# Kernel optimization log

Measured on AMD Instinct MI355X. Metric: run time of the kernel, lower is better.

The kernel has to match this reference:

```python
import jax, jax.numpy as jnp
import numpy as np

DIM = 64
PATCH = 8
KH = KW = 7
K = KH * KW
PAD = 3


def conv2d(x, w, pad):
    return jax.lax.conv_general_dilated(
        x, w, window_strides=(1, 1), padding=[(pad, pad), (pad, pad)],
        dimension_numbers=('NCHW', 'OIHW', 'NCHW'))


def deform_conv2d(x, offset, mask, weight):
    # torchvision modulated deformable conv v2, stride=1, dilation=1, pad=PAD
    B, C, H, W = x.shape
    off = offset.reshape(B, K, 2, H, W)  # channel pairs are (dy, dx)
    ky, kx = jnp.meshgrid(jnp.arange(KH), jnp.arange(KW), indexing='ij')
    ky = ky.reshape(K).astype(x.dtype)
    kx = kx.reshape(K).astype(x.dtype)
    hh = jnp.arange(H, dtype=x.dtype)
    ww = jnp.arange(W, dtype=x.dtype)
    # sampling locations: p0 - pad + p_k + offset, shape [B,K,H,W]
    y = hh[None, None, :, None] - PAD + ky[None, :, None, None] + off[:, :, 0]
    xx = ww[None, None, None, :] - PAD + kx[None, :, None, None] + off[:, :, 1]

    y0 = jnp.floor(y)
    x0 = jnp.floor(xx)
    wy = y - y0
    wx = xx - x0

    img_flat = x.reshape(B, C, H * W)

    def gather(yi, xi):
        valid = (yi >= 0) & (yi < H) & (xi >= 0) & (xi < W)
        yc = jnp.clip(yi, 0, H - 1).astype(jnp.int32)
        xc = jnp.clip(xi, 0, W - 1).astype(jnp.int32)
        lin = (yc * W + xc).reshape(B, -1)  # [B, K*H*W]
        v = jax.vmap(lambda im, idx: im[:, idx])(img_flat, lin)  # [B,C,K*H*W]
        v = v.reshape(B, C, K, H, W)
        return v * valid[:, None].astype(x.dtype)

    val = ((1 - wy) * (1 - wx))[:, None] * gather(y0, x0) \
        + ((1 - wy) * wx)[:, None] * gather(y0, x0 + 1) \
        + (wy * (1 - wx))[:, None] * gather(y0 + 1, x0) \
        + (wy * wx)[:, None] * gather(y0 + 1, x0 + 1)
    val = val * mask[:, None]  # modulation, [B,C,K,H,W]
    wf = weight.reshape(weight.shape[0], weight.shape[1], K)
    return jnp.einsum('bckhw,ock->bohw', val, wf)


def setup_inputs() -> dict:
    key = jax.random.key(0)
    ks = jax.random.split(key, 12)
    B, C, H, W = 1, DIM, 192, 192
    s = 0.05
    return {
        'enc': jax.random.normal(ks[0], (B, C, H, W), jnp.float32),
        'dec': jax.random.normal(ks[1], (B, C, H, W), jnp.float32),
        'inverse_offset': jax.random.normal(ks[2], (B, 2 * K, H, W), jnp.float32),
        'inverse_weight': jax.random.uniform(ks[3], (B, K, H, W), jnp.float32),
        'w_proj_in': jax.random.normal(ks[4], (C, C, 1, 1), jnp.float32) * s,
        'fft_w': 1.0 + 0.1 * jax.random.normal(ks[5], (C, 1, 1, PATCH, PATCH // 2 + 1), jnp.float32),
        'w_proj_out': jax.random.normal(ks[6], (2 * C, 2 * C, 1, 1), jnp.float32) * s,
        'w_deform': jax.random.normal(ks[7], (C, C, KH, KW), jnp.float32) * s,
        'w_conv1': jax.random.normal(ks[8], (C, C, 1, 1), jnp.float32) * s,
        'w_conv2': jax.random.normal(ks[9], (C, C, 3, 3), jnp.float32) * s,
    }


def reference(enc, dec, inverse_offset, inverse_weight, w_proj_in, fft_w,
              w_proj_out, w_deform, w_conv1, w_conv2):
    B, C, h, w = enc.shape
    reverse = deform_conv2d(enc, inverse_offset, inverse_weight, w_deform)
    reverse = conv2d(reverse, w_conv1, 0)

    e = conv2d(enc, w_proj_in, 0)
    # check_image_size: pad H,W to multiples of PATCH (no-op for 192)
    ph = (-h) % PATCH
    pw = (-w) % PATCH
    e = jnp.pad(e, ((0, 0), (0, 0), (0, ph), (0, pw)))
    Hp, Wp = h + ph, w + pw
    # [B,C,h',w',p1,p2]
    xp = e.reshape(B, C, Hp // PATCH, PATCH, Wp // PATCH, PATCH).transpose(0, 1, 2, 4, 3, 5)
    xf = jnp.fft.rfft2(xp.astype(jnp.float32)) * fft_w  # fft_w [C,1,1,8,5] broadcasts
    xp = jnp.fft.irfft2(xf, s=(PATCH, PATCH))
    e = xp.transpose(0, 1, 2, 4, 3, 5).reshape(B, C, Hp, Wp)[:, :, :h, :w]

    e = e + reverse
    e = conv2d(e, w_conv2, 1)
    feat = jnp.concatenate([e, dec], axis=1)
    feat = conv2d(feat, w_proj_out, 0)
    x1, x2 = jnp.split(feat, 2, axis=1)  # SimpleGate
    return x1 * x2
```

## Files before the change

kernel.cpp:

```cpp
#include <hip/hip_runtime.h>
#include <math.h>

#define CH    64
#define WW    192
#define HH    192
#define HWSZ  (192*192)
#define KK    49
#define ROWP  68
#define SROW  72
#define C3ROW 72
#define OROW  136

typedef __attribute__((ext_vector_type(8))) short     s16x8;
typedef __attribute__((ext_vector_type(8))) _Float16  h16x8;
typedef __attribute__((ext_vector_type(2))) _Float16  h16x2;
typedef __attribute__((ext_vector_type(2))) __fp16    fp16x2;
typedef __attribute__((ext_vector_type(4))) float     f32x4;

__device__ __forceinline__ unsigned short f2h(float f) {
    union { _Float16 h; unsigned short s; } u; u.h = (_Float16)f;
    return u.s;
}

__device__ __forceinline__ unsigned pkh(float lo, float hi) {
    union { fp16x2 h; unsigned u; } v;
    v.h = __builtin_amdgcn_cvt_pkrtz(lo, hi);
    return v.u;
}

__device__ __forceinline__ h16x2 cvt2h(float a) {
    union { fp16x2 h; h16x2 o; } v;
    v.h = __builtin_amdgcn_cvt_pkrtz(a, a);
    return v.o;
}

__device__ __forceinline__ h16x2 as_h2(unsigned u) {
    union { unsigned u; h16x2 h; } v; v.u = u; return v.h;
}

__device__ __forceinline__ unsigned as_u(h16x2 h) {
    union { h16x2 h; unsigned u; } v; v.h = h; return v.u;
}

__device__ const float c_cos8[8] = {
    1.f, 0.70710678118654752f, 0.f, -0.70710678118654752f,
   -1.f, -0.70710678118654752f, 0.f, 0.70710678118654752f };

__global__ __launch_bounds__(256) void k_prep(
    const float* __restrict__ fw,
    const float* __restrict__ wd,
    const float* __restrict__ w2,
    const float* __restrict__ wc1,
    const float* __restrict__ wpo,
    const float* __restrict__ wpi,
    float* __restrict__ krT,
    short* __restrict__ wA,
    short* __restrict__ w2A,
    short* __restrict__ wpoA,
    short* __restrict__ wpiA)
{
    int tid = blockIdx.x * blockDim.x + threadIdx.x;
    int nt  = gridDim.x * blockDim.x;
    for (int t = tid; t < 64 * 64; t += nt) {
        int uv = t >> 6, c = t & 63;
        int u = uv >> 3, v = uv & 7;
        float acc = 0.f;
        for (int ky = 0; ky < 8; ky++)
            for (int kx = 0; kx < 8; kx++) {
                float wv = (kx <= 4) ? fw[c * 40 + ky * 5 + kx]
                                     : fw[c * 40 + ((8 - ky) & 7) * 5 + (8 - kx)];
                acc += wv * c_cos8[(ky * u + kx * v) & 7];
            }
        krT[uv * 64 + c] = acc * (1.f / 64.f);
    }
    for (int t = tid; t < 9 * 4096; t += nt) {
        int tap = t / 4096, rem = t & 4095;
        int o = rem >> 6, c = rem & 63;
        float v = w2[(o * 64 + c) * 9 + tap];
        int fi = tap * 8 + (o >> 4) * 2 + (c >> 5);
        int ln = ((c >> 3) & 3) * 16 + (o & 15);
        w2A[fi * 512 + ln * 8 + (c & 7)] = (short)f2h(v);
    }
    for (int t = tid; t < 128 * 128; t += nt) {
        int o = t >> 7, c = t & 127;
        int fi = (o >> 4) * 4 + (c >> 5);
        int ln = ((c >> 3) & 3) * 16 + (o & 15);
        wpoA[fi * 512 + ln * 8 + (c & 7)] = (short)f2h(wpo[t]);
    }
    for (int t = tid; t < 64 * 64; t += nt) {
        int o = t >> 6, c = t & 63;
        int fi = (o >> 4) * 2 + (c >> 5);
        int ln = ((c >> 3) & 3) * 16 + (o & 15);
        wpiA[fi * 512 + ln * 8 + (c & 7)] = (short)f2h(wpi[t]);
    }

    __shared__ float wdk [64 * ROWP];
    __shared__ float wc1s[64 * ROWP];
    int k = blockIdx.x;
    int t = threadIdx.x;
#pragma unroll
    for (int r = 0; r < 16; r++) {
        int idx = t + r * 256;
        int o = idx >> 6, c = idx & 63;
        wdk [o * ROWP + c] = wd[(o * 64 + c) * KK + k];
        wc1s[o * ROWP + c] = wc1[o * 64 + c];
    }
    __syncthreads();

    int ot = (t >> 4) * 4, cb = (t & 15) * 4;
    float a[4][4];
#pragma unroll
    for (int i = 0; i < 4; i++)
#pragma unroll
        for (int j = 0; j < 4; j++) a[i][j] = 0.f;
    for (int o = 0; o < 64; o++) {
        float wv_[4], sv_[4];
#pragma unroll
        for (int i = 0; i < 4; i++) wv_[i] = wc1s[(ot + i) * ROWP + o];
#pragma unroll
        for (int j = 0; j < 4; j++) sv_[j] = wdk[o * ROWP + cb + j];
#pragma unroll
        for (int i = 0; i < 4; i++)
#pragma unroll
            for (int j = 0; j < 4; j++) a[i][j] += wv_[i] * sv_[j];
    }
#pragma unroll
    for (int i = 0; i < 4; i++)
#pragma unroll
        for (int j = 0; j < 4; j++) {
            int o2 = ot + i, c = cb + j;
            int tt = o2 >> 4, m = o2 & 15;
            int kt = c >> 5, q = (c >> 3) & 3, jj = c & 7;
            int ln = q * 16 + m;
            wA[(k * 8 + tt * 2 + kt) * 512 + ln * 8 + jj] = (short)f2h(a[i][j]);
        }
}

__global__ __launch_bounds__(256) void k_trans(
    const float* __restrict__ enc, unsigned short* __restrict__ encH)
{
    __shared__ float s[64 * 65];
    int t = threadIdx.x;
    int base = blockIdx.x * 64;
#pragma unroll
    for (int r = 0; r < 16; r++) {
        int idx = t + r * 256;
        int p = idx & 63, c = idx >> 6;
        s[p * 65 + c] = enc[c * HWSZ + base + p];
    }
    __syncthreads();
#pragma unroll
    for (int r = 0; r < 8; r++) {
        int idx = t + r * 256;
        int pr = idx & 31, p = idx >> 5;
        ((unsigned*)encH)[(base + p) * 32 + pr] =
            pkh(s[p * 65 + 2 * pr], s[p * 65 + 2 * pr + 1]);
    }
}

#define REDW 20

__global__ __launch_bounds__(256) void k_deform(
    const unsigned short* __restrict__ encH, const float* __restrict__ off,
    const float* __restrict__ msk, const short* __restrict__ wA,
    float* __restrict__ rev)
{
    __shared__ __align__(16) short sm[4][16 * SROW];
    __shared__ __align__(16) float red[2 * 64 * REDW];

    int t = threadIdx.x;
    int lane = t & 63, w = t >> 6;
    int b = blockIdx.x;
    int xcd = b & 7, blk = b >> 3;
    int gy  = xcd * 24 + blk / 12;
    int gx0 = (blk % 12) * 16;

    int sp = lane >> 2, g = lane & 3;
    int sgx  = gx0 + sp;
    int gp_s = gy * WW + sgx;
    int n = lane & 15, q = lane >> 4;
    short* smw = &sm[w][0];

    f32x4 acc[4];
#pragma unroll
    for (int ot = 0; ot < 4; ot++) acc[ot] = (f32x4){0.f, 0.f, 0.f, 0.f};

    int kstart = (w == 0) ? 0 : 13 + (w - 1) * 12;
    int kend   = (w == 0) ? 13 : kstart + 12;

    float dy = off[(2 * kstart) * HWSZ + gp_s];
    float dx = off[(2 * kstart + 1) * HWSZ + gp_s];
    float mm = msk[kstart * HWSZ + gp_s];

#pragma unroll 1
    for (int k = kstart; k < kend; k++) {
        int ky = k / 7, kx = k % 7;
        float y = (float)(gy  - 3 + ky) + dy;
        float x = (float)(sgx - 3 + kx) + dx;
        float y0f = floorf(y), x0f = floorf(x);
        float wy = y - y0f, wx = x - x0f;
        int iy0 = (int)y0f, ix0 = (int)x0f;
        int iy1 = iy0 + 1, ix1 = ix0 + 1;
        bool vy0 = (iy0 >= 0) & (iy0 < HH);
        bool vy1 = (iy1 >= 0) & (iy1 < HH);
        bool vx0 = (ix0 >= 0) & (ix0 < WW);
        bool vx1 = (ix1 >= 0) & (ix1 < WW);
        int iy0c = min(max(iy0, 0), HH - 1), iy1c = min(max(iy1, 0), HH - 1);
        int ix0c = min(max(ix0, 0), WW - 1), ix1c = min(max(ix1, 0), WW - 1);
        float a00 = (vy0 & vx0) ? (1.f - wy) * (1.f - wx) * mm : 0.f;
        float a01 = (vy0 & vx1) ? (1.f - wy) * wx * mm : 0.f;
        float a10 = (vy1 & vx0) ? wy * (1.f - wx) * mm : 0.f;
        float a11 = (vy1 & vx1) ? wy * wx * mm : 0.f;

        const unsigned short* b00p = encH + (iy0c * WW + ix0c) * 64 + g * 8;
        const unsigned short* b01p = encH + (iy0c * WW + ix1c) * 64 + g * 8;
        const unsigned short* b10p = encH + (iy1c * WW + ix0c) * 64 + g * 8;
        const unsigned short* b11p = encH + (iy1c * WW + ix1c) * 64 + g * 8;
        uint4 u00[2], u01[2], u10[2], u11[2];
        u00[0] = *(const uint4*)b00p;  u00[1] = *(const uint4*)(b00p + 32);
        u01[0] = *(const uint4*)b01p;  u01[1] = *(const uint4*)(b01p + 32);
        u10[0] = *(const uint4*)b10p;  u10[1] = *(const uint4*)(b10p + 32);
        u11[0] = *(const uint4*)b11p;  u11[1] = *(const uint4*)(b11p + 32);

        float dyn = 0.f, dxn = 0.f, mmn = 0.f;
        if (k + 1 < kend) {
            dyn = off[(2 * k + 2) * HWSZ + gp_s];
            dxn = off[(2 * k + 3) * HWSZ + gp_s];
            mmn = msk[(k + 1) * HWSZ + gp_s];
        }

        h16x8 af[8];
#pragma unroll
        for (int f = 0; f < 8; f++)
            af[f] = *(const h16x8*)&wA[(k * 8 + f) * 512 + lane * 8];

        h16x2 w00 = cvt2h(a00);
        h16x2 w01 = cvt2h(a01);
        h16x2 w10 = cvt2h(a10);
        h16x2 w11 = cvt2h(a11);

        unsigned c00[8] = {u00[0].x, u00[0].y, u00[0].z, u00[0].w,
                           u00[1].x, u00[1].y, u00[1].z, u00[1].w};
        unsigned c01[8] = {u01[0].x, u01[0].y, u01[0].z, u01[0].w,
                           u01[1].x, u01[1].y, u01[1].z, u01[1].w};
        unsigned c10[8] = {u10[0].x, u10[0].y, u10[0].z, u10[0].w,
                           u10[1].x, u10[1].y, u10[1].z, u10[1].w};
        unsigned c11[8] = {u11[0].x, u11[0].y, u11[0].z, u11[0].w,
                           u11[1].x, u11[1].y, u11[1].z, u11[1].w};
        unsigned pk[8];
#pragma unroll
        for (int j = 0; j < 8; j++) {
            h16x2 r = as_h2(c00[j]) * w00;
            r = as_h2(c01[j]) * w01 + r;
            r = as_h2(c10[j]) * w10 + r;
            r = as_h2(c11[j]) * w11 + r;
            pk[j] = as_u(r);
        }
        *(uint4*)&smw[sp * SROW + g * 8]      = make_uint4(pk[0], pk[1], pk[2], pk[3]);
        *(uint4*)&smw[sp * SROW + 32 + g * 8] = make_uint4(pk[4], pk[5], pk[6], pk[7]);

        h16x8 b0 = *(const h16x8*)&smw[n * SROW +  0 + q * 8];
        h16x8 b1 = *(const h16x8*)&smw[n * SROW + 32 + q * 8];

#pragma unroll
        for (int ot = 0; ot < 4; ot++) {
            acc[ot] = __builtin_amdgcn_mfma_f32_16x16x32_f16(af[ot * 2],     b0, acc[ot], 0, 0, 0);
            acc[ot] = __builtin_amdgcn_mfma_f32_16x16x32_f16(af[ot * 2 + 1], b1, acc[ot], 0, 0, 0);
        }

        dy = dyn; dx = dxn; mm = mmn;
    }

    if (w >= 2) {
        float* rp = &red[((w - 2) * 64 + lane) * REDW];
#pragma unroll
        for (int ot = 0; ot < 4; ot++)
            *(float4*)&rp[ot * 4] = make_float4(acc[ot][0], acc[ot][1], acc[ot][2], acc[ot][3]);
    }
    __syncthreads();
    if (w < 2) {
        const float* rp = &red[(w * 64 + lane) * REDW];
#pragma unroll
        for (int ot = 0; ot < 4; ot++) {
            float4 v = *(const float4*)&rp[ot * 4];
            acc[ot][0] += v.x; acc[ot][1] += v.y;
            acc[ot][2] += v.z; acc[ot][3] += v.w;
        }
    }
    __syncthreads();
    if (w == 1) {
        float* rp = &red[lane * REDW];
#pragma unroll
        for (int ot = 0; ot < 4; ot++)
            *(float4*)&rp[ot * 4] = make_float4(acc[ot][0], acc[ot][1], acc[ot][2], acc[ot][3]);
    }
    __syncthreads();
    if (w == 0) {
        const float* rp = &red[lane * REDW];
#pragma unroll
        for (int ot = 0; ot < 4; ot++) {
            float4 v = *(const float4*)&rp[ot * 4];
            acc[ot][0] += v.x; acc[ot][1] += v.y;
            acc[ot][2] += v.z; acc[ot][3] += v.w;
        }
        int gp_m = gy * WW + gx0 + n;
#pragma unroll
        for (int ot = 0; ot < 4; ot++) {
            float4 rv = make_float4(acc[ot][0], acc[ot][1], acc[ot][2], acc[ot][3]);
            *(float4*)&rev[gp_m * 64 + ot * 16 + q * 4] = rv;
        }
    }
}

__global__ __launch_bounds__(256) void k_fft(
    const unsigned short* __restrict__ encH, const short* __restrict__ wpiA,
    const float* __restrict__ krT, float* __restrict__ e1)
{
    __shared__ __align__(16) short sbf[64 * SROW];
    __shared__ __align__(16) float e0[64 * ROWP];
    int t = threadIdx.x;
    int pbx = blockIdx.x % 24, pby = blockIdx.x / 24;
    int gx0 = pbx * 8, gy0 = pby * 8;

#pragma unroll
    for (int r = 0; r < 2; r++) {
        int idx = t + r * 256;
        int px = idx >> 3, g8 = idx & 7;
        int gy = gy0 + (px >> 3), gx = gx0 + (px & 7);
        *(uint4*)&sbf[px * SROW + g8 * 8] =
            *(const uint4*)&encH[(gy * WW + gx) * 64 + g8 * 8];
    }
    __syncthreads();

    int lane = t & 63, w = t >> 6;
    int n = lane & 15, q = lane >> 4;
    h16x8 a0 = *(const h16x8*)&wpiA[(w * 2 + 0) * 512 + lane * 8];
    h16x8 a1 = *(const h16x8*)&wpiA[(w * 2 + 1) * 512 + lane * 8];
#pragma unroll
    for (int j = 0; j < 4; j++) {
        h16x8 b0 = *(const h16x8*)&sbf[(j * 16 + n) * SROW +  0 + q * 8];
        h16x8 b1 = *(const h16x8*)&sbf[(j * 16 + n) * SROW + 32 + q * 8];
        f32x4 acc = {0.f, 0.f, 0.f, 0.f};
        acc = __builtin_amdgcn_mfma_f32_16x16x32_f16(a0, b0, acc, 0, 0, 0);
        acc = __builtin_amdgcn_mfma_f32_16x16x32_f16(a1, b1, acc, 0, 0, 0);
#pragma unroll
        for (int r = 0; r < 4; r++)
            e0[(j * 16 + n) * ROWP + w * 16 + q * 4 + r] = acc[r];
    }
    __syncthreads();

    int o = t & 63;
    int yb = t >> 6;
#pragma unroll
    for (int yy = 0; yy < 2; yy++) {
        int y = yb + yy * 4;
        float outr[8];
#pragma unroll
        for (int x = 0; x < 8; x++) outr[x] = 0.f;
#pragma unroll
        for (int u = 0; u < 8; u++) {
            int ry = (y - u + 8) & 7;
            float row[8];
#pragma unroll
            for (int rx = 0; rx < 8; rx++)
                row[rx] = e0[(ry * 8 + rx) * ROWP + o];
#pragma unroll
            for (int v = 0; v < 8; v++) {
                float kv = krT[(u * 8 + v) * 64 + o];
#pragma unroll
                for (int x = 0; x < 8; x++)
                    outr[x] += kv * row[(x - v + 8) & 7];
            }
        }
        int gy = gy0 + y;
#pragma unroll
        for (int x = 0; x < 8; x++)
            e1[(gy * WW + gx0 + x) * 64 + o] = outr[x];
    }
}

__global__ __launch_bounds__(256) void k_c3out(
    const float* __restrict__ e1, const float* __restrict__ rev,
    const short* __restrict__ w2A, const float* __restrict__ dec,
    const short* __restrict__ wpoA, float* __restrict__ out)
{
    __shared__ __align__(16) short sm[4][54 * C3ROW];
    int t = threadIdx.x;
    int lane = t & 63, w = t >> 6;
    int b = blockIdx.x;
    int xcd = b & 7, blk = b >> 3;
    int gy  = xcd * 24 + blk / 3;
    int gx0 = (blk % 3) * 64 + w * 16;
    short* smw = &sm[w][0];
    int n = lane & 15, q = lane >> 4;

    for (int r = 0; r < 14; r++) {
        int u = lane + r * 64;
        if (u < 864) {
            int rp = u >> 4, g = u & 15;
            int row = rp / 18, pxl = rp - row * 18;
            int gyy = gy + row - 1, gxx = gx0 + pxl - 1;
            float4 v = make_float4(0.f, 0.f, 0.f, 0.f);
            if (gyy >= 0 && gyy < HH && gxx >= 0 && gxx < WW) {
                int gp = (gyy * WW + gxx) * 64 + g * 4;
                float4 va = *(const float4*)&e1[gp];
                float4 vb = *(const float4*)&rev[gp];
                v.x = va.x + vb.x; v.y = va.y + vb.y;
                v.z = va.z + vb.z; v.w = va.w + vb.w;
            }
            *(uint2*)&smw[rp * C3ROW + g * 4] = make_uint2(pkh(v.x, v.y), pkh(v.z, v.w));
        }
    }

    f32x4 acc[4];
#pragma unroll
    for (int ot = 0; ot < 4; ot++) acc[ot] = (f32x4){0.f, 0.f, 0.f, 0.f};

#pragma unroll 1
    for (int tap = 0; tap < 9; tap++) {
        int dy = tap / 3, dx = tap - dy * 3;
        int rp = dy * 18 + n + dx;
        h16x8 b0 = *(const h16x8*)&smw[rp * C3ROW +  0 + q * 8];
        h16x8 b1 = *(const h16x8*)&smw[rp * C3ROW + 32 + q * 8];
#pragma unroll
        for (int ot = 0; ot < 4; ot++) {
            h16x8 a0 = *(const h16x8*)&w2A[(tap * 8 + ot * 2 + 0) * 512 + lane * 8];
            h16x8 a1 = *(const h16x8*)&w2A[(tap * 8 + ot * 2 + 1) * 512 + lane * 8];
            acc[ot] = __builtin_amdgcn_mfma_f32_16x16x32_f16(a0, b0, acc[ot], 0, 0, 0);
            acc[ot] = __builtin_amdgcn_mfma_f32_16x16x32_f16(a1, b1, acc[ot], 0, 0, 0);
        }
    }

#pragma unroll
    for (int ot = 0; ot < 4; ot++) {
        unsigned lo = pkh(acc[ot][0], acc[ot][1]);
        unsigned hi = pkh(acc[ot][2], acc[ot][3]);
        *(uint2*)&smw[n * OROW + ot * 16 + q * 4] = make_uint2(lo, hi);
    }
    {
        int gp = gy * WW + gx0 + n;
        unsigned pk[8];
#pragma unroll
        for (int i = 0; i < 8; i++) {
            float va = dec[(q * 16 + 2 * i)     * HWSZ + gp];
            float vb = dec[(q * 16 + 2 * i + 1) * HWSZ + gp];
            pk[i] = pkh(va, vb);
        }
        *(uint4*)&smw[n * OROW + 64 + q * 16]     = make_uint4(pk[0], pk[1], pk[2], pk[3]);
        *(uint4*)&smw[n * OROW + 64 + q * 16 + 8] = make_uint4(pk[4], pk[5], pk[6], pk[7]);
    }

    f32x4 go[8];
#pragma unroll
    for (int ot = 0; ot < 8; ot++) go[ot] = (f32x4){0.f, 0.f, 0.f, 0.f};

#pragma unroll 1
    for (int kt = 0; kt < 4; kt++) {
        h16x8 bb = *(const h16x8*)&smw[n * OROW + kt * 32 + q * 8];
#pragma unroll
        for (int ot = 0; ot < 8; ot++) {
            h16x8 aa = *(const h16x8*)&wpoA[(ot * 4 + kt) * 512 + lane * 8];
            go[ot] = __builtin_amdgcn_mfma_f32_16x16x32_f16(aa, bb, go[ot], 0, 0, 0);
        }
    }

    int gp = gy * WW + gx0 + n;
#pragma unroll
    for (int ot = 0; ot < 4; ot++)
#pragma unroll
        for (int r = 0; r < 4; r++)
            out[(ot * 16 + q * 4 + r) * HWSZ + gp] = go[ot][r] * go[ot + 4][r];
}

extern "C" void kernel_launch(void* const* d_in, const int* in_sizes, int n_in,
                              void* d_out, int out_size, void* d_ws, size_t ws_size,
                              hipStream_t stream)
{
    const float* enc  = (const float*)d_in[0];
    const float* dec  = (const float*)d_in[1];
    const float* ioff = (const float*)d_in[2];
    const float* iwt  = (const float*)d_in[3];
    const float* wpi  = (const float*)d_in[4];
    const float* fw   = (const float*)d_in[5];
    const float* wpo  = (const float*)d_in[6];
    const float* wd   = (const float*)d_in[7];
    const float* wc1  = (const float*)d_in[8];
    const float* wc2  = (const float*)d_in[9];
    float* out = (float*)d_out;
    float* ws  = (float*)d_ws;

    float*          krT  = ws;
    float*          rev  = ws + 4096;
    float*          e1   = ws + 2363392;
    unsigned short* encH = (unsigned short*)(ws + 4722688);
    short*          wA   = (short*)(ws + 5902336);
    short*          w2A  = (short*)(ws + 6002688);
    short*          wpoA = (short*)(ws + 6021120);
    short*          wpiA = (short*)(ws + 6029312);

    hipLaunchKernelGGL(k_prep,   dim3(49),   dim3(256), 0, stream,
                       fw, wd, wc2, wc1, wpo, wpi, krT, wA, w2A, wpoA, wpiA);
    hipLaunchKernelGGL(k_trans,  dim3(576),  dim3(256), 0, stream, enc, encH);
    hipLaunchKernelGGL(k_deform, dim3(2304), dim3(256), 0, stream, encH, ioff, iwt, wA, rev);
    hipLaunchKernelGGL(k_fft,    dim3(576),  dim3(256), 0, stream, encH, wpiA, krT, e1);
    hipLaunchKernelGGL(k_c3out,  dim3(576),  dim3(256), 0, stream, e1, rev, w2A, dec, wpoA, out);
}
```

Baseline: 214.7 us.

## Double-buffer deformable gather loads to overlap next tap with current MFMA

Restructures the deformable-conv tap loop into a two-stage software pipeline. The bilinear corner gathers for tap k+1 are issued into a second register set before tap k's blend and MFMAs run, so gather latency can hide behind compute. It also makes each lane load 16 contiguous channels instead of two 8-channel chunks 32 apart, and writes them to shared memory in the same natural channel order. In exchange it roughly doubles the registers held for gathered data, which could lower occupancy.

```diff
diff --git a/kernel.cpp b/kernel.cpp
--- a/kernel.cpp
+++ b/kernel.cpp
@@ -160,6 +160,80 @@
 
 #define REDW 20
 
+#define ISSUE_TAP(KK_, DY_, DX_, MM_, A00_, A01_, A10_, A11_, C0_, C1_, C2_, C3_) \
+    do {                                                                       \
+        int ky_ = (KK_) / 7, kx_ = (KK_) % 7;                                  \
+        float y_ = (float)(gy  - 3 + ky_) + (DY_);                             \
+        float x_ = (float)(sgx - 3 + kx_) + (DX_);                             \
+        float y0f_ = floorf(y_), x0f_ = floorf(x_);                            \
+        float wy_ = y_ - y0f_, wx_ = x_ - x0f_;                                \
+        int iy0_ = (int)y0f_, ix0_ = (int)x0f_;                                \
+        int iy1_ = iy0_ + 1, ix1_ = ix0_ + 1;                                  \
+        bool vy0_ = (iy0_ >= 0) & (iy0_ < HH);                                 \
+        bool vy1_ = (iy1_ >= 0) & (iy1_ < HH);                                 \
+        bool vx0_ = (ix0_ >= 0) & (ix0_ < WW);                                 \
+        bool vx1_ = (ix1_ >= 0) & (ix1_ < WW);                                 \
+        int iy0c_ = min(max(iy0_, 0), HH - 1), iy1c_ = min(max(iy1_, 0), HH - 1); \
+        int ix0c_ = min(max(ix0_, 0), WW - 1), ix1c_ = min(max(ix1_, 0), WW - 1); \
+        A00_ = (vy0_ & vx0_) ? (1.f - wy_) * (1.f - wx_) * (MM_) : 0.f;        \
+        A01_ = (vy0_ & vx1_) ? (1.f - wy_) * wx_ * (MM_) : 0.f;                \
+        A10_ = (vy1_ & vx0_) ? wy_ * (1.f - wx_) * (MM_) : 0.f;                \
+        A11_ = (vy1_ & vx1_) ? wy_ * wx_ * (MM_) : 0.f;                        \
+        const unsigned short* p00_ = encH + (iy0c_ * WW + ix0c_) * 64 + g * 16; \
+        const unsigned short* p01_ = encH + (iy0c_ * WW + ix1c_) * 64 + g * 16; \
+        const unsigned short* p10_ = encH + (iy1c_ * WW + ix0c_) * 64 + g * 16; \
+        const unsigned short* p11_ = encH + (iy1c_ * WW + ix1c_) * 64 + g * 16; \
+        C0_[0] = *(const uint4*)p00_;  C0_[1] = *(const uint4*)(p00_ + 8);     \
+        C1_[0] = *(const uint4*)p01_;  C1_[1] = *(const uint4*)(p01_ + 8);     \
+        C2_[0] = *(const uint4*)p10_;  C2_[1] = *(const uint4*)(p10_ + 8);     \
+        C3_[0] = *(const uint4*)p11_;  C3_[1] = *(const uint4*)(p11_ + 8);     \
+    } while (0)
+
+#define CONSUME_TAP(KK_, A00_, A01_, A10_, A11_, C0_, C1_, C2_, C3_)           \
+    do {                                                                       \
+        h16x8 af_[8];                                                          \
+        _Pragma("unroll")                                                      \
+        for (int f = 0; f < 8; f++)                                            \
+            af_[f] = *(const h16x8*)&wA[((KK_) * 8 + f) * 512 + lane * 8];     \
+        h16x2 w00_ = cvt2h(A00_), w01_ = cvt2h(A01_);                          \
+        h16x2 w10_ = cvt2h(A10_), w11_ = cvt2h(A11_);                          \
+        unsigned c00_[8] = {C0_[0].x, C0_[0].y, C0_[0].z, C0_[0].w,            \
+                            C0_[1].x, C0_[1].y, C0_[1].z, C0_[1].w};           \
+        unsigned c01_[8] = {C1_[0].x, C1_[0].y, C1_[0].z, C1_[0].w,            \
+                            C1_[1].x, C1_[1].y, C1_[1].z, C1_[1].w};           \
+        unsigned c10_[8] = {C2_[0].x, C2_[0].y, C2_[0].z, C2_[0].w,            \
+                            C2_[1].x, C2_[1].y, C2_[1].z, C2_[1].w};           \
+        unsigned c11_[8] = {C3_[0].x, C3_[0].y, C3_[0].z, C3_[0].w,            \
+                            C3_[1].x, C3_[1].y, C3_[1].z, C3_[1].w};           \
+        unsigned pk_[8];                                                       \
+        _Pragma("unroll")                                                      \
+        for (int j = 0; j < 8; j++) {                                          \
+            h16x2 r_ = as_h2(c00_[j]) * w00_;                                  \
+            r_ = as_h2(c01_[j]) * w01_ + r_;                                   \
+            r_ = as_h2(c10_[j]) * w10_ + r_;                                   \
+            r_ = as_h2(c11_[j]) * w11_ + r_;                                   \
+            pk_[j] = as_u(r_);                                                 \
+        }                                                                      \
+        *(uint4*)&smw[sp * SROW + g * 16]     = make_uint4(pk_[0], pk_[1], pk_[2], pk_[3]); \
+        *(uint4*)&smw[sp * SROW + g * 16 + 8] = make_uint4(pk_[4], pk_[5], pk_[6], pk_[7]); \
+        h16x8 b0_ = *(const h16x8*)&smw[n * SROW +  0 + q * 8];                \
+        h16x8 b1_ = *(const h16x8*)&smw[n * SROW + 32 + q * 8];                \
+        _Pragma("unroll")                                                      \
+        for (int ot = 0; ot < 4; ot++) {                                       \
+            acc[ot] = __builtin_amdgcn_mfma_f32_16x16x32_f16(af_[ot * 2],     b0_, acc[ot], 0, 0, 0); \
+            acc[ot] = __builtin_amdgcn_mfma_f32_16x16x32_f16(af_[ot * 2 + 1], b1_, acc[ot], 0, 0, 0); \
+        }                                                                      \
+    } while (0)
+
+#define LOAD_OFF(J_)                                                           \
+    do {                                                                       \
+        if ((J_) < kend) {                                                     \
+            dy = off[(2 * (J_)) * HWSZ + gp_s];                                \
+            dx = off[(2 * (J_) + 1) * HWSZ + gp_s];                            \
+            mm = msk[(J_) * HWSZ + gp_s];                                      \
+        }                                                                      \
+    } while (0)
+
 __global__ __launch_bounds__(256) void k_deform(
     const unsigned short* __restrict__ encH, const float* __restrict__ off,
     const float* __restrict__ msk, const short* __restrict__ wA,
@@ -192,83 +266,28 @@
     float dx = off[(2 * kstart + 1) * HWSZ + gp_s];
     float mm = msk[kstart * HWSZ + gp_s];
 
+    float aA00, aA01, aA10, aA11;
+    float aB00, aB01, aB10, aB11;
+    uint4 cA0[2], cA1[2], cA2[2], cA3[2];
+    uint4 cB0[2], cB1[2], cB2[2], cB3[2];
+
+    ISSUE_TAP(kstart, dy, dx, mm, aA00, aA01, aA10, aA11, cA0, cA1, cA2, cA3);
+    LOAD_OFF(kstart + 1);
+
 #pragma unroll 1
-    for (int k = kstart; k < kend; k++) {
-        int ky = k / 7, kx = k % 7;
-        float y = (float)(gy  - 3 + ky) + dy;
-        float x = (float)(sgx - 3 + kx) + dx;
-        float y0f = floorf(y), x0f = floorf(x);
-        float wy = y - y0f, wx = x - x0f;
-        int iy0 = (int)y0f, ix0 = (int)x0f;
-        int iy1 = iy0 + 1, ix1 = ix0 + 1;
-        bool vy0 = (iy0 >= 0) & (iy0 < HH);
-        bool vy1 = (iy1 >= 0) & (iy1 < HH);
-        bool vx0 = (ix0 >= 0) & (ix0 < WW);
-        bool vx1 = (ix1 >= 0) & (ix1 < WW);
-        int iy0c = min(max(iy0, 0), HH - 1), iy1c = min(max(iy1, 0), HH - 1);
-        int ix0c = min(max(ix0, 0), WW - 1), ix1c = min(max(ix1, 0), WW - 1);
-        float a00 = (vy0 & vx0) ? (1.f - wy) * (1.f - wx) * mm : 0.f;
-        float a01 = (vy0 & vx1) ? (1.f - wy) * wx * mm : 0.f;
-        float a10 = (vy1 & vx0) ? wy * (1.f - wx) * mm : 0.f;
-        float a11 = (vy1 & vx1) ? wy * wx * mm : 0.f;
-
-        const unsigned short* b00p = encH + (iy0c * WW + ix0c) * 64 + g * 8;
-        const unsigned short* b01p = encH + (iy0c * WW + ix1c) * 64 + g * 8;
-        const unsigned short* b10p = encH + (iy1c * WW + ix0c) * 64 + g * 8;
-        const unsigned short* b11p = encH + (iy1c * WW + ix1c) * 64 + g * 8;
-        uint4 u00[2], u01[2], u10[2], u11[2];
-        u00[0] = *(const uint4*)b00p;  u00[1] = *(const uint4*)(b00p + 32);
-        u01[0] = *(const uint4*)b01p;  u01[1] = *(const uint4*)(b01p + 32);
-        u10[0] = *(const uint4*)b10p;  u10[1] = *(const uint4*)(b10p + 32);
-        u11[0] = *(const uint4*)b11p;  u11[1] = *(const uint4*)(b11p + 32);
-
-        float dyn = 0.f, dxn = 0.f, mmn = 0.f;
+    for (int k = kstart; k < kend; k += 2) {
         if (k + 1 < kend) {
-            dyn = off[(2 * k + 2) * HWSZ + gp_s];
-            dxn = off[(2 * k + 3) * HWSZ + gp_s];
-            mmn = msk[(k + 1) * HWSZ + gp_s];
-        }
-
-        h16x8 af[8];
-#pragma unroll
-        for (int f = 0; f < 8; f++)
-            af[f] = *(const h16x8*)&wA[(k * 8 + f) * 512 + lane * 8];
-
-        h16x2 w00 = cvt2h(a00);
-        h16x2 w01 = cvt2h(a01);
-        h16x2 w10 = cvt2h(a10);
-        h16x2 w11 = cvt2h(a11);
-
-        unsigned c00[8] = {u00[0].x, u00[0].y, u00[0].z, u00[0].w,
-                           u00[1].x, u00[1].y, u00[1].z, u00[1].w};
-        unsigned c01[8] = {u01[0].x, u01[0].y, u01[0].z, u01[0].w,
-                           u01[1].x, u01[1].y, u01[1].z, u01[1].w};
-        unsigned c10[8] = {u10[0].x, u10[0].y, u10[0].z, u10[0].w,
-                           u10[1].x, u10[1].y, u10[1].z, u10[1].w};
-        unsigned c11[8] = {u11[0].x, u11[0].y, u11[0].z, u11[0].w,
-                           u11[1].x, u11[1].y, u11[1].z, u11[1].w};
-        unsigned pk[8];
-#pragma unroll
-        for (int j = 0; j < 8; j++) {
-            h16x2 r = as_h2(c00[j]) * w00;
-            r = as_h2(c01[j]) * w01 + r;
-            r = as_h2(c10[j]) * w10 + r;
-            r = as_h2(c11[j]) * w11 + r;
-            pk[j] = as_u(r);
-        }
-        *(uint4*)&smw[sp * SROW + g * 8]      = make_uint4(pk[0], pk[1], pk[2], pk[3]);
-        *(uint4*)&smw[sp * SROW + 32 + g * 8] = make_uint4(pk[4], pk[5], pk[6], pk[7]);
-
-        h16x8 b0 = *(const h16x8*)&smw[n * SROW +  0 + q * 8];
-        h16x8 b1 = *(const h16x8*)&smw[n * SROW + 32 + q * 8];
-
-#pragma unroll
-        for (int ot = 0; ot < 4; ot++) {
-            acc[ot] = __builtin_amdgcn_mfma_f32_16x16x32_f16(af[ot * 2],     b0, acc[ot], 0, 0, 0);
-            acc[ot] = __builtin_amdgcn_mfma_f32_16x16x32_f16(af[ot * 2 + 1], b1, acc[ot], 0, 0, 0);
-        }
-
-        dy = dyn; dx = dxn; mm = mmn;
+            ISSUE_TAP(k + 1, dy, dx, mm, aB00, aB01, aB10, aB11, cB0, cB1, cB2, cB3);
+            LOAD_OFF(k + 2);
+        }
+        CONSUME_TAP(k, aA00, aA01, aA10, aA11, cA0, cA1, cA2, cA3);
+        if (k + 1 < kend) {
+            if (k + 2 < kend) {
+                ISSUE_TAP(k + 2, dy, dx, mm, aA00, aA01, aA10, aA11, cA0, cA1, cA2, cA3);
+                LOAD_OFF(k + 3);
+            }
+            CONSUME_TAP(k + 1, aB00, aB01, aB10, aB11, cB0, cB1, cB2, cB3);
+        }
     }
 
     if (w >= 2) {
```

After: 226.0 us. +5.2%, slower.
